# Kernel optimization log

Hardware: AMD Instinct MI355X
Metric: run time of the kernel (lower is better)

Reference implementation:

```python
import jax, jax.numpy as jnp
import numpy as np

N_NODES = 50000
N_EDGES = 800000
IN_CH = 128
HID = 64
HEADS = 4
OUT_CH = 64
NEG_SLOPE = 0.2


def _add_self_loops(ei, n):
    loops = jnp.tile(jnp.arange(n, dtype=ei.dtype)[None, :], (2, 1))
    return jnp.concatenate([ei, loops], axis=1)


def _gat_conv(x, ei, W, a_s, a_d, b, concat):
    """PyG-style GATConv. x:[N,F], ei:[2,E], W:[F,H*C], a_s/a_d:[H,C]."""
    N = x.shape[0]
    H, C = a_s.shape
    h = (x @ W).reshape(N, H, C)                     # [N,H,C]
    src, dst = ei[0], ei[1]
    al_s = (h * a_s[None]).sum(-1)                   # [N,H]
    al_d = (h * a_d[None]).sum(-1)                   # [N,H]
    logits = jax.nn.leaky_relu(al_s[src] + al_d[dst], NEG_SLOPE)  # [E,H]
    # segment softmax over incoming edges of each dst node
    m = jax.ops.segment_max(logits, dst, num_segments=N)
    m = jax.lax.stop_gradient(jnp.where(jnp.isfinite(m), m, 0.0))
    ex = jnp.exp(logits - m[dst])
    denom = jax.ops.segment_sum(ex, dst, num_segments=N)
    alpha = ex / (denom[dst] + 1e-16)                # [E,H]
    out = jax.ops.segment_sum(alpha[:, :, None] * h[src], dst, num_segments=N)  # [N,H,C]
    out = out.reshape(N, H * C) if concat else out.mean(axis=1)
    return out + b


def _hetero_layer(x, edges, self_loop_flags, W, a_s, a_d, b, concat):
    N = x.shape[0]
    out = None
    for r in range(3):
        ei = _add_self_loops(edges[r], N) if self_loop_flags[r] else edges[r]
        o = _gat_conv(x, ei, W[r], a_s[r], a_d[r], b[r], concat)
        out = o if out is None else out + o
    return out


def setup_inputs() -> dict:
    key = jax.random.key(0)
    ks = jax.random.split(key, 16)
    s = 0.05
    return {
        "x": jax.random.normal(ks[0], (N_NODES, IN_CH), jnp.float32),
        "e_blocks": jax.random.randint(ks[1], (2, N_EDGES), 0, N_NODES),
        "e_spatial": jax.random.randint(ks[2], (2, N_EDGES), 0, N_NODES),
        "e_similar": jax.random.randint(ks[3], (2, N_EDGES), 0, N_NODES),
        "W1": jax.random.normal(ks[4], (3, IN_CH, HEADS * HID), jnp.float32) * s,
        "a1s": jax.random.normal(ks[5], (3, HEADS, HID), jnp.float32) * s,
        "a1d": jax.random.normal(ks[6], (3, HEADS, HID), jnp.float32) * s,
        "b1": jax.random.normal(ks[7], (3, HEADS * HID), jnp.float32) * s,
        "W2": jax.random.normal(ks[8], (3, HEADS * HID, HEADS * HID), jnp.float32) * s,
        "a2s": jax.random.normal(ks[9], (3, HEADS, HID), jnp.float32) * s,
        "a2d": jax.random.normal(ks[10], (3, HEADS, HID), jnp.float32) * s,
        "b2": jax.random.normal(ks[11], (3, HID), jnp.float32) * s,
        "Wl": jax.random.normal(ks[12], (HID, OUT_CH), jnp.float32) * s,
        "bl": jax.random.normal(ks[13], (OUT_CH,), jnp.float32) * s,
    }


def reference(x, e_blocks, e_spatial, e_similar, W1, a1s, a1d, b1,
              W2, a2s, a2d, b2, Wl, bl):
    edges = [e_blocks, e_spatial, e_similar]
    self_loops = [False, True, True]  # 'blocks' has add_self_loops=False
    h = _hetero_layer(x, edges, self_loops, W1, a1s, a1d, b1, concat=True)
    h = jax.nn.relu(h)
    h = _hetero_layer(h, edges, self_loops, W2, a2s, a2d, b2, concat=False)
    h = jax.nn.relu(h)
    return h @ Wl + bl
```

## Files before the change

kernel.cpp:

```cpp
#include <hip/hip_runtime.h>
#include <hip/hip_bf16.h>
#include <hip/hip_fp16.h>

#define NN 50000
#define NE 800000
#define FIN 128
#define HCC 256
#define OC 64
#define NSL 0.2f
#define NT3 (3 * NN)

typedef __attribute__((ext_vector_type(8))) short sh8;
typedef __attribute__((ext_vector_type(16))) float f32x16;

struct __attribute__((aligned(8))) h4 { __half x, y, z, w; };

__device__ __forceinline__ unsigned short bf_rne(float f) {
  unsigned u = __float_as_uint(f);
  u += 0x7FFF + ((u >> 16) & 1);
  return (unsigned short)(u >> 16);
}

__device__ __forceinline__ float edge_w(float lg) {
  lg = (lg > 0.f) ? lg : NSL * lg;
  return __expf(lg);
}

template<int KK>
__global__ __launch_bounds__(256) void k_prep(const float* __restrict__ W,
                                              short* __restrict__ out) {
  int i = blockIdx.x * 256 + threadIdx.x;
  if (i >= 3 * KK * 256) return;
  int r = i / (KK * 256);
  int rem = i - r * KK * 256;
  int k = rem >> 8;
  int n = rem & 255;
  float f = W[i];
  unsigned short hb = bf_rne(f);
  float hf = __uint_as_float(((unsigned)hb) << 16);
  unsigned short lb = bf_rne(f - hf);
  int cb = n >> 7, c = n & 127, ks8 = k >> 3, kj = k & 7;
  size_t base = (size_t)r * 4 * KK * 128;
  size_t oh = base + ((size_t)((cb * 2 + 0) * (KK / 8) + ks8) * 128 + c) * 8 + kj;
  size_t ol = base + ((size_t)((cb * 2 + 1) * (KK / 8) + ks8) * 128 + c) * 8 + kj;
  out[oh] = (short)hb;
  out[ol] = (short)lb;
}

__global__ void k_hist(const int* __restrict__ dst, int* __restrict__ deg, int n) {
  int i = blockIdx.x * blockDim.x + threadIdx.x;
  int st = gridDim.x * blockDim.x;
  for (; i < n; i += st) atomicAdd(&deg[dst[i]], 1);
}

__global__ __launch_bounds__(1024) void k_bsum(const int* __restrict__ deg3,
                                               int* __restrict__ bsum) {
  __shared__ int s[1024];
  int t = threadIdx.x;
  int i = blockIdx.x * 1024 + t;
  s[t] = (i < NT3) ? deg3[i] : 0;
  __syncthreads();
  for (int off = 512; off > 0; off >>= 1) {
    if (t < off) s[t] += s[t + off];
    __syncthreads();
  }
  if (t == 0) bsum[blockIdx.x] = s[0];
}

__global__ __launch_bounds__(256) void k_scan2(const int* __restrict__ bsum,
                                               int* __restrict__ boffs, int nb) {
  __shared__ int s[256];
  int t = threadIdx.x;
  int v = (t < nb) ? bsum[t] : 0;
  s[t] = v;
  __syncthreads();
  for (int off = 1; off < 256; off <<= 1) {
    int x = (t >= off) ? s[t - off] : 0;
    __syncthreads();
    s[t] += x;
    __syncthreads();
  }
  if (t < nb) boffs[t] = s[t] - v;
}

__global__ __launch_bounds__(1024) void k_rowptr(const int* __restrict__ deg3,
                                                 const int* __restrict__ boffs,
                                                 int* __restrict__ rpA,
                                                 int* __restrict__ cursor3) {
  __shared__ int s[1024];
  int t = threadIdx.x;
  int i = blockIdx.x * 1024 + t;
  int d = (i < NT3) ? deg3[i] : 0;
  s[t] = d;
  __syncthreads();
  for (int off = 1; off < 1024; off <<= 1) {
    int x = (t >= off) ? s[t - off] : 0;
    __syncthreads();
    s[t] += x;
    __syncthreads();
  }
  if (i < NT3) {
    int excl = boffs[blockIdx.x] + s[t] - d;
    int r = (i < NN) ? 0 : ((i < 2 * NN) ? 1 : 2);
    int n = i - r * NN;
    int val = excl - r * NE;
    rpA[r * (NN + 1) + n] = val;
    cursor3[i] = val;
  }
  if (blockIdx.x == 0 && t < 3) rpA[t * (NN + 1) + NN] = NE;
}

__global__ void k_scatter(const int* __restrict__ srcv, const int* __restrict__ dstv,
                          int* __restrict__ cursor, int* __restrict__ csr_src, int n) {
  int i = blockIdx.x * blockDim.x + threadIdx.x;
  int st = gridDim.x * blockDim.x;
  for (; i < n; i += st) {
    int pos = atomicAdd(&cursor[dstv[i]], 1);
    csr_src[pos] = srcv[i];
  }
}

template<int KK, bool RELU>
__global__ __launch_bounds__(256) void k_mgemm(const float* __restrict__ A,
                                               const short* __restrict__ Bc,
                                               const float* __restrict__ asf,
                                               const float* __restrict__ adf,
                                               __half* __restrict__ hout,
                                               float* __restrict__ als,
                                               float* __restrict__ ald, int M) {
  const int tid = threadIdx.x;
  const int lane = tid & 63;
  const int w = tid >> 6;
  const int l31 = lane & 31;
  const int lg = lane >> 5;
  const int wrow = blockIdx.x * 64 + (w & 1) * 32;
  const int ch = w >> 1;

  f32x16 acc[4];
#pragma unroll
  for (int t = 0; t < 4; ++t) acc[t] = (f32x16)(0.f);

  const int r = wrow + l31;
  const bool aok = r < M;
  const float* ap = A + (size_t)r * KK;
  const short* bh = Bc + (size_t)(ch * 2 + 0) * KK * 128 + l31 * 8;
  const short* bl = Bc + (size_t)(ch * 2 + 1) * KK * 128 + l31 * 8;

#pragma unroll 2
  for (int kst = 0; kst < KK / 16; ++kst) {
    const int k0 = kst * 16 + lg * 8;
    float4 x0 = make_float4(0.f, 0.f, 0.f, 0.f), x1 = x0;
    if (aok) {
      x0 = *(const float4*)(ap + k0);
      x1 = *(const float4*)(ap + k0 + 4);
    }
    const int ks8 = kst * 2 + lg;
    const short* bhp = bh + (size_t)ks8 * 1024;
    const short* blp = bl + (size_t)ks8 * 1024;
    sh8 bhf[4], blf[4];
#pragma unroll
    for (int t = 0; t < 4; ++t) {
      bhf[t] = *(const sh8*)(bhp + t * 256);
      blf[t] = *(const sh8*)(blp + t * 256);
    }
    float fa[8] = {x0.x, x0.y, x0.z, x0.w, x1.x, x1.y, x1.z, x1.w};
    sh8 ahi, alo;
#pragma unroll
    for (int j = 0; j < 8; ++j) {
      float f = fa[j];
      if (RELU) f = fmaxf(f, 0.f);
      unsigned short hb = bf_rne(f);
      float hf = __uint_as_float(((unsigned)hb) << 16);
      unsigned short lb = bf_rne(f - hf);
      ahi[j] = (short)hb;
      alo[j] = (short)lb;
    }
#pragma unroll
    for (int t = 0; t < 4; ++t) {
      acc[t] = __builtin_amdgcn_mfma_f32_32x32x16_bf16(ahi, bhf[t], acc[t], 0, 0, 0);
      acc[t] = __builtin_amdgcn_mfma_f32_32x32x16_bf16(alo, bhf[t], acc[t], 0, 0, 0);
      acc[t] = __builtin_amdgcn_mfma_f32_32x32x16_bf16(ahi, blf[t], acc[t], 0, 0, 0);
    }
  }

  float asr[4], adr[4];
#pragma unroll
  for (int t = 0; t < 4; ++t) {
    int col = ch * 128 + t * 32 + l31;
    asr[t] = asf[col];
    adr[t] = adf[col];
  }
#pragma unroll
  for (int v = 0; v < 16; ++v) {
    const int rl = (v & 3) + 8 * (v >> 2) + 4 * lg;
    const int row = wrow + rl;
    const bool rok = row < M;
    float s0 = 0.f, s1 = 0.f, d0 = 0.f, d1 = 0.f;
    __half* hp = hout + (size_t)row * 256 + ch * 128 + l31;
#pragma unroll
    for (int t = 0; t < 4; ++t) {
      float dv = acc[t][v];
      if (rok) hp[t * 32] = __float2half(dv);
      if (t < 2) { s0 += dv * asr[t]; d0 += dv * adr[t]; }
      else       { s1 += dv * asr[t]; d1 += dv * adr[t]; }
    }
#pragma unroll
    for (int m = 1; m < 32; m <<= 1) {
      s0 += __shfl_xor(s0, m);
      s1 += __shfl_xor(s1, m);
      d0 += __shfl_xor(d0, m);
      d1 += __shfl_xor(d1, m);
    }
    if (rok && l31 == 0) {
      *(float2*)(als + (size_t)row * 4 + ch * 2) = make_float2(s0, s1);
      *(float2*)(ald + (size_t)row * 4 + ch * 2) = make_float2(d0, d1);
    }
  }
}

template<bool CONCAT, bool SELFLOOP, bool FIRST>
__global__ __launch_bounds__(256) void k_gather(const __half* __restrict__ h,
                                                const float* __restrict__ als,
                                                const float* __restrict__ ald,
                                                const int* __restrict__ row_ptr,
                                                const int* __restrict__ csr_src,
                                                const float* __restrict__ bias,
                                                float* __restrict__ outp) {
  int gid = blockIdx.x * blockDim.x + threadIdx.x;
  int n = gid >> 6;
  int lane = threadIdx.x & 63;
  if (n >= NN) return;
  int head = lane >> 4;
  float ad = ald[n * 4 + head];
  int rs = row_ptr[n];
  int re = row_ptr[n + 1];
  float ax = 0.f, ay = 0.f, az = 0.f, aw = 0.f;
  float wsum = 0.f;
  const size_t loff = (size_t)lane * 4;

  int i = rs;
  for (; i + 4 <= re; i += 4) {
    int s0 = csr_src[i], s1 = csr_src[i + 1], s2 = csr_src[i + 2], s3 = csr_src[i + 3];
    float al0 = als[s0 * 4 + head];
    float al1 = als[s1 * 4 + head];
    float al2 = als[s2 * 4 + head];
    float al3 = als[s3 * 4 + head];
    h4 v0 = *(const h4*)&h[(size_t)s0 * HCC + loff];
    h4 v1 = *(const h4*)&h[(size_t)s1 * HCC + loff];
    h4 v2 = *(const h4*)&h[(size_t)s2 * HCC + loff];
    h4 v3 = *(const h4*)&h[(size_t)s3 * HCC + loff];
    float w0 = edge_w(al0 + ad), w1 = edge_w(al1 + ad);
    float w2 = edge_w(al2 + ad), w3 = edge_w(al3 + ad);
    wsum += (w0 + w1) + (w2 + w3);
    ax = fmaf(w0, __half2float(v0.x), ax); ay = fmaf(w0, __half2float(v0.y), ay);
    az = fmaf(w0, __half2float(v0.z), az); aw = fmaf(w0, __half2float(v0.w), aw);
    ax = fmaf(w1, __half2float(v1.x), ax); ay = fmaf(w1, __half2float(v1.y), ay);
    az = fmaf(w1, __half2float(v1.z), az); aw = fmaf(w1, __half2float(v1.w), aw);
    ax = fmaf(w2, __half2float(v2.x), ax); ay = fmaf(w2, __half2float(v2.y), ay);
    az = fmaf(w2, __half2float(v2.z), az); aw = fmaf(w2, __half2float(v2.w), aw);
    ax = fmaf(w3, __half2float(v3.x), ax); ay = fmaf(w3, __half2float(v3.y), ay);
    az = fmaf(w3, __half2float(v3.z), az); aw = fmaf(w3, __half2float(v3.w), aw);
  }
  for (; i < re; ++i) {
    int s = csr_src[i];
    float w = edge_w(als[s * 4 + head] + ad);
    wsum += w;
    h4 hv = *(const h4*)&h[(size_t)s * HCC + loff];
    ax = fmaf(w, __half2float(hv.x), ax);
    ay = fmaf(w, __half2float(hv.y), ay);
    az = fmaf(w, __half2float(hv.z), az);
    aw = fmaf(w, __half2float(hv.w), aw);
  }
  if (SELFLOOP) {
    float w = edge_w(als[n * 4 + head] + ad);
    wsum += w;
    h4 hv = *(const h4*)&h[(size_t)n * HCC + loff];
    ax = fmaf(w, __half2float(hv.x), ax);
    ay = fmaf(w, __half2float(hv.y), ay);
    az = fmaf(w, __half2float(hv.z), az);
    aw = fmaf(w, __half2float(hv.w), aw);
  }
  float inv = 1.0f / (wsum + 1e-16f);
  if (CONCAT) {
    size_t base = (size_t)n * HCC + lane * 4;
    float4 bb = *(const float4*)&bias[lane * 4];
    float4 o;
    if (FIRST) {
      o.x = ax * inv + bb.x;
      o.y = ay * inv + bb.y;
      o.z = az * inv + bb.z;
      o.w = aw * inv + bb.w;
    } else {
      o = *(float4*)&outp[base];
      o.x += ax * inv + bb.x;
      o.y += ay * inv + bb.y;
      o.z += az * inv + bb.z;
      o.w += aw * inv + bb.w;
    }
    *(float4*)&outp[base] = o;
  } else {
    float vx = ax * inv, vy = ay * inv, vz = az * inv, vw = aw * inv;
    vx += __shfl_xor(vx, 16); vy += __shfl_xor(vy, 16);
    vz += __shfl_xor(vz, 16); vw += __shfl_xor(vw, 16);
    vx += __shfl_xor(vx, 32); vy += __shfl_xor(vy, 32);
    vz += __shfl_xor(vz, 32); vw += __shfl_xor(vw, 32);
    if (lane < 16) {
      size_t base = (size_t)n * OC + lane * 4;
      float4 bb = *(const float4*)&bias[lane * 4];
      float4 o;
      if (FIRST) {
        o.x = 0.25f * vx + bb.x;
        o.y = 0.25f * vy + bb.y;
        o.z = 0.25f * vz + bb.z;
        o.w = 0.25f * vw + bb.w;
      } else {
        o = *(float4*)&outp[base];
        o.x += 0.25f * vx + bb.x;
        o.y += 0.25f * vy + bb.y;
        o.z += 0.25f * vz + bb.z;
        o.w += 0.25f * vw + bb.w;
      }
      *(float4*)&outp[base] = o;
    }
  }
}

__global__ __launch_bounds__(256) void k_final(const float* __restrict__ out2,
                                               const float* __restrict__ Wl,
                                               const float* __restrict__ bl,
                                               float* __restrict__ outp) {
  __shared__ float Ws[64 * 64];
  __shared__ float bs[64];
  int tid = threadIdx.x;
  for (int i = tid; i < 4096; i += 256) Ws[i] = Wl[i];
  if (tid < 64) bs[tid] = bl[tid];
  __syncthreads();
  int r = blockIdx.x * 4 + (tid >> 6);
  int c = tid & 63;
  if (r >= NN) return;
  const float* xr = &out2[(size_t)r * OC];
  float acc = bs[c];
#pragma unroll
  for (int k = 0; k < 64; ++k) {
    float xv = xr[k];
    xv = (xv > 0.f) ? xv : 0.f;
    acc = fmaf(xv, Ws[k * 64 + c], acc);
  }
  outp[(size_t)r * OC + c] = acc;
}

extern "C" void kernel_launch(void* const* d_in, const int* in_sizes, int n_in,
                              void* d_out, int out_size, void* d_ws, size_t ws_size,
                              hipStream_t stream) {
  const float* x   = (const float*)d_in[0];
  const int* e_b   = (const int*)d_in[1];
  const int* e_sp  = (const int*)d_in[2];
  const int* e_si  = (const int*)d_in[3];
  const float* W1  = (const float*)d_in[4];
  const float* a1s = (const float*)d_in[5];
  const float* a1d = (const float*)d_in[6];
  const float* b1  = (const float*)d_in[7];
  const float* W2  = (const float*)d_in[8];
  const float* a2s = (const float*)d_in[9];
  const float* a2d = (const float*)d_in[10];
  const float* b2  = (const float*)d_in[11];
  const float* Wl  = (const float*)d_in[12];
  const float* bl  = (const float*)d_in[13];
  float* out = (float*)d_out;

  char* ws = (char*)d_ws;
  size_t off = 0;
  auto alloc = [&](size_t b) {
    char* p = ws + off;
    off += (b + 255) & ~(size_t)255;
    return p;
  };
  __half* h   = (__half*)alloc((size_t)NN * HCC * 2);
  float* out1 = (float*)alloc((size_t)NN * HCC * 4);
  float* out2 = (float*)alloc((size_t)NN * OC * 4);
  float* als  = (float*)alloc((size_t)NN * 4 * 4);
  float* ald  = (float*)alloc((size_t)NN * 4 * 4);
  int* deg3   = (int*)alloc((size_t)NT3 * 4);
  int* cursor3= (int*)alloc((size_t)NT3 * 4);
  int* rpA    = (int*)alloc((size_t)3 * (NN + 1) * 4);
  int* bsum   = (int*)alloc(256 * 4);
  int* boffs  = (int*)alloc(256 * 4);
  short* Wc1  = (short*)alloc((size_t)3 * 4 * FIN * 128 * 2);
  short* Wc2  = (short*)alloc((size_t)3 * 4 * HCC * 128 * 2);
  int* cs[3];
  for (int r = 0; r < 3; ++r) cs[r] = (int*)alloc((size_t)NE * 4);

  const int* edges[3] = {e_b, e_sp, e_si};

  k_prep<FIN><<<(3 * FIN * 256 + 255) / 256, 256, 0, stream>>>(W1, Wc1);
  k_prep<HCC><<<(3 * HCC * 256 + 255) / 256, 256, 0, stream>>>(W2, Wc2);

  hipMemsetAsync(deg3, 0, (size_t)NT3 * 4, stream);
  for (int r = 0; r < 3; ++r)
    k_hist<<<1024, 256, 0, stream>>>(edges[r] + NE, deg3 + r * NN, NE);
  const int NB = (NT3 + 1023) / 1024;
  k_bsum<<<NB, 1024, 0, stream>>>(deg3, bsum);
  k_scan2<<<1, 256, 0, stream>>>(bsum, boffs, NB);
  k_rowptr<<<NB, 1024, 0, stream>>>(deg3, boffs, rpA, cursor3);
  for (int r = 0; r < 3; ++r)
    k_scatter<<<1024, 256, 0, stream>>>(edges[r], edges[r] + NE, cursor3 + r * NN, cs[r], NE);

  const int gblocks = (NN + 63) / 64;
  const int ablocks = (NN * 64) / 256;

  for (int r = 0; r < 3; ++r) {
    k_mgemm<FIN, false><<<gblocks, 256, 0, stream>>>(
        x, Wc1 + (size_t)r * 4 * FIN * 128,
        a1s + r * HCC, a1d + r * HCC, h, als, ald, NN);
    if (r == 0)
      k_gather<true, false, true><<<ablocks, 256, 0, stream>>>(h, als, ald, rpA + r * (NN + 1), cs[r], b1 + r * HCC, out1);
    else
      k_gather<true, true, false><<<ablocks, 256, 0, stream>>>(h, als, ald, rpA + r * (NN + 1), cs[r], b1 + r * HCC, out1);
  }
  for (int r = 0; r < 3; ++r) {
    k_mgemm<HCC, true><<<gblocks, 256, 0, stream>>>(
        out1, Wc2 + (size_t)r * 4 * HCC * 128,
        a2s + r * HCC, a2d + r * HCC, h, als, ald, NN);
    if (r == 0)
      k_gather<false, false, true><<<ablocks, 256, 0, stream>>>(h, als, ald, rpA + r * (NN + 1), cs[r], b2 + r * OC, out2);
    else
      k_gather<false, true, false><<<ablocks, 256, 0, stream>>>(h, als, ald, rpA + r * (NN + 1), cs[r], b2 + r * OC, out2);
  }
  k_final<<<(NN + 3) / 4, 256, 0, stream>>>(out2, Wl, bl, out);
}
```

Baseline: 1.001 ms.

## Batch three relations per layer into single GEMM and fused gather kernels

The GEMMs for all three relations now run in one launch, with blockIdx.y selecting the relation, and write into a per-relation h buffer. A single gather kernel then aggregates all three relations per node in registers and adds all biases, which removes the read-modify-write of the float output between relations. The layer-1 output is stored as fp16 with ReLU applied, halving the bytes the second GEMM reads. The cost is more workspace for the tripled h and attention buffers, and some precision loss from storing the intermediate activation in fp16.

```diff
diff --git a/kernel.cpp b/kernel.cpp
--- a/kernel.cpp
+++ b/kernel.cpp
@@ -11,6 +11,7 @@
 #define NT3 (3 * NN)
 
 typedef __attribute__((ext_vector_type(8))) short sh8;
+typedef __attribute__((ext_vector_type(8))) unsigned short u16x8;
 typedef __attribute__((ext_vector_type(16))) float f32x16;
 
 struct __attribute__((aligned(8))) h4 { __half x, y, z, w; };
@@ -19,6 +20,11 @@
   unsigned u = __float_as_uint(f);
   u += 0x7FFF + ((u >> 16) & 1);
   return (unsigned short)(u >> 16);
+}
+
+__device__ __forceinline__ float hbits2f(unsigned short u) {
+  __half_raw hr; hr.x = u;
+  return __half2float((__half)hr);
 }
 
 __device__ __forceinline__ float edge_w(float lg) {
@@ -120,14 +126,22 @@
   }
 }
 
-template<int KK, bool RELU>
-__global__ __launch_bounds__(256) void k_mgemm(const float* __restrict__ A,
-                                               const short* __restrict__ Bc,
-                                               const float* __restrict__ asf,
-                                               const float* __restrict__ adf,
-                                               __half* __restrict__ hout,
-                                               float* __restrict__ als,
-                                               float* __restrict__ ald, int M) {
+template<int KK, bool AF32>
+__global__ __launch_bounds__(256) void k_mgemm(const void* __restrict__ Av,
+                                               const short* __restrict__ BcAll,
+                                               const float* __restrict__ asfAll,
+                                               const float* __restrict__ adfAll,
+                                               __half* __restrict__ houtAll,
+                                               float* __restrict__ alsAll,
+                                               float* __restrict__ aldAll, int M) {
+  const int rel = blockIdx.y;
+  const short* Bc = BcAll + (size_t)rel * 4 * KK * 128;
+  const float* asf = asfAll + rel * HCC;
+  const float* adf = adfAll + rel * HCC;
+  __half* hout = houtAll + (size_t)rel * NN * HCC;
+  float* als = alsAll + (size_t)rel * NN * 4;
+  float* ald = aldAll + (size_t)rel * NN * 4;
+
   const int tid = threadIdx.x;
   const int lane = tid & 63;
   const int w = tid >> 6;
@@ -142,17 +156,28 @@
 
   const int r = wrow + l31;
   const bool aok = r < M;
-  const float* ap = A + (size_t)r * KK;
+  const float* apf = (const float*)Av + (size_t)r * KK;
+  const __half* aph = (const __half*)Av + (size_t)r * KK;
   const short* bh = Bc + (size_t)(ch * 2 + 0) * KK * 128 + l31 * 8;
   const short* bl = Bc + (size_t)(ch * 2 + 1) * KK * 128 + l31 * 8;
 
 #pragma unroll 2
   for (int kst = 0; kst < KK / 16; ++kst) {
     const int k0 = kst * 16 + lg * 8;
-    float4 x0 = make_float4(0.f, 0.f, 0.f, 0.f), x1 = x0;
-    if (aok) {
-      x0 = *(const float4*)(ap + k0);
-      x1 = *(const float4*)(ap + k0 + 4);
+    float fa[8];
+    if (AF32) {
+      float4 x0 = make_float4(0.f, 0.f, 0.f, 0.f), x1 = x0;
+      if (aok) {
+        x0 = *(const float4*)(apf + k0);
+        x1 = *(const float4*)(apf + k0 + 4);
+      }
+      fa[0] = x0.x; fa[1] = x0.y; fa[2] = x0.z; fa[3] = x0.w;
+      fa[4] = x1.x; fa[5] = x1.y; fa[6] = x1.z; fa[7] = x1.w;
+    } else {
+      u16x8 hv = {0, 0, 0, 0, 0, 0, 0, 0};
+      if (aok) hv = *(const u16x8*)(aph + k0);
+#pragma unroll
+      for (int j = 0; j < 8; ++j) fa[j] = hbits2f(hv[j]);
     }
     const int ks8 = kst * 2 + lg;
     const short* bhp = bh + (size_t)ks8 * 1024;
@@ -163,12 +188,10 @@
       bhf[t] = *(const sh8*)(bhp + t * 256);
       blf[t] = *(const sh8*)(blp + t * 256);
     }
-    float fa[8] = {x0.x, x0.y, x0.z, x0.w, x1.x, x1.y, x1.z, x1.w};
     sh8 ahi, alo;
 #pragma unroll
     for (int j = 0; j < 8; ++j) {
       float f = fa[j];
-      if (RELU) f = fmaxf(f, 0.f);
       unsigned short hb = bf_rne(f);
       float hf = __uint_as_float(((unsigned)hb) << 16);
       unsigned short lb = bf_rne(f - hf);
@@ -218,29 +241,20 @@
   }
 }
 
-template<bool CONCAT, bool SELFLOOP, bool FIRST>
-__global__ __launch_bounds__(256) void k_gather(const __half* __restrict__ h,
-                                                const float* __restrict__ als,
-                                                const float* __restrict__ ald,
-                                                const int* __restrict__ row_ptr,
-                                                const int* __restrict__ csr_src,
-                                                const float* __restrict__ bias,
-                                                float* __restrict__ outp) {
-  int gid = blockIdx.x * blockDim.x + threadIdx.x;
-  int n = gid >> 6;
-  int lane = threadIdx.x & 63;
-  if (n >= NN) return;
-  int head = lane >> 4;
+template<bool SL>
+__device__ __forceinline__ void gat_rel(int n, int head, size_t loff,
+                                        const __half* __restrict__ h,
+                                        const float* __restrict__ als,
+                                        const float* __restrict__ ald,
+                                        const int* __restrict__ rp,
+                                        const int* __restrict__ cs,
+                                        float& ox, float& oy, float& oz, float& ow) {
   float ad = ald[n * 4 + head];
-  int rs = row_ptr[n];
-  int re = row_ptr[n + 1];
-  float ax = 0.f, ay = 0.f, az = 0.f, aw = 0.f;
-  float wsum = 0.f;
-  const size_t loff = (size_t)lane * 4;
-
+  int rs = rp[n], re = rp[n + 1];
+  float ax = 0.f, ay = 0.f, az = 0.f, aw = 0.f, wsum = 0.f;
   int i = rs;
   for (; i + 4 <= re; i += 4) {
-    int s0 = csr_src[i], s1 = csr_src[i + 1], s2 = csr_src[i + 2], s3 = csr_src[i + 3];
+    int s0 = cs[i], s1 = cs[i + 1], s2 = cs[i + 2], s3 = cs[i + 3];
     float al0 = als[s0 * 4 + head];
     float al1 = als[s1 * 4 + head];
     float al2 = als[s2 * 4 + head];
@@ -262,7 +276,7 @@
     az = fmaf(w3, __half2float(v3.z), az); aw = fmaf(w3, __half2float(v3.w), aw);
   }
   for (; i < re; ++i) {
-    int s = csr_src[i];
+    int s = cs[i];
     float w = edge_w(als[s * 4 + head] + ad);
     wsum += w;
     h4 hv = *(const h4*)&h[(size_t)s * HCC + loff];
@@ -271,7 +285,7 @@
     az = fmaf(w, __half2float(hv.z), az);
     aw = fmaf(w, __half2float(hv.w), aw);
   }
-  if (SELFLOOP) {
+  if (SL) {
     float w = edge_w(als[n * 4 + head] + ad);
     wsum += w;
     h4 hv = *(const h4*)&h[(size_t)n * HCC + loff];
@@ -281,46 +295,60 @@
     aw = fmaf(w, __half2float(hv.w), aw);
   }
   float inv = 1.0f / (wsum + 1e-16f);
+  ox = fmaf(ax, inv, ox);
+  oy = fmaf(ay, inv, oy);
+  oz = fmaf(az, inv, oz);
+  ow = fmaf(aw, inv, ow);
+}
+
+template<bool CONCAT>
+__global__ __launch_bounds__(256) void k_gather3(const __half* __restrict__ h3,
+                                                 const float* __restrict__ als3,
+                                                 const float* __restrict__ ald3,
+                                                 const int* __restrict__ rpA,
+                                                 const int* __restrict__ cs0,
+                                                 const int* __restrict__ cs1,
+                                                 const int* __restrict__ cs2,
+                                                 const float* __restrict__ bias,
+                                                 __half* __restrict__ o16,
+                                                 float* __restrict__ o32) {
+  int gid = blockIdx.x * blockDim.x + threadIdx.x;
+  int n = gid >> 6;
+  int lane = threadIdx.x & 63;
+  if (n >= NN) return;
+  int head = lane >> 4;
+  size_t loff = (size_t)lane * 4;
+  const size_t HS = (size_t)NN * HCC;
+  const size_t AS = (size_t)NN * 4;
+  float ox = 0.f, oy = 0.f, oz = 0.f, ow = 0.f;
+  gat_rel<false>(n, head, loff, h3,          als3,          ald3,          rpA,               cs0, ox, oy, oz, ow);
+  gat_rel<true >(n, head, loff, h3 + HS,     als3 + AS,     ald3 + AS,     rpA + (NN + 1),    cs1, ox, oy, oz, ow);
+  gat_rel<true >(n, head, loff, h3 + 2 * HS, als3 + 2 * AS, ald3 + 2 * AS, rpA + 2 * (NN + 1), cs2, ox, oy, oz, ow);
   if (CONCAT) {
-    size_t base = (size_t)n * HCC + lane * 4;
-    float4 bb = *(const float4*)&bias[lane * 4];
-    float4 o;
-    if (FIRST) {
-      o.x = ax * inv + bb.x;
-      o.y = ay * inv + bb.y;
-      o.z = az * inv + bb.z;
-      o.w = aw * inv + bb.w;
-    } else {
-      o = *(float4*)&outp[base];
-      o.x += ax * inv + bb.x;
-      o.y += ay * inv + bb.y;
-      o.z += az * inv + bb.z;
-      o.w += aw * inv + bb.w;
-    }
-    *(float4*)&outp[base] = o;
+    float4 b0 = *(const float4*)&bias[lane * 4];
+    float4 b1 = *(const float4*)&bias[HCC + lane * 4];
+    float4 b2 = *(const float4*)&bias[2 * HCC + lane * 4];
+    h4 o;
+    o.x = __float2half(fmaxf(ox + b0.x + b1.x + b2.x, 0.f));
+    o.y = __float2half(fmaxf(oy + b0.y + b1.y + b2.y, 0.f));
+    o.z = __float2half(fmaxf(oz + b0.z + b1.z + b2.z, 0.f));
+    o.w = __float2half(fmaxf(ow + b0.w + b1.w + b2.w, 0.f));
+    *(h4*)&o16[(size_t)n * HCC + loff] = o;
   } else {
-    float vx = ax * inv, vy = ay * inv, vz = az * inv, vw = aw * inv;
-    vx += __shfl_xor(vx, 16); vy += __shfl_xor(vy, 16);
-    vz += __shfl_xor(vz, 16); vw += __shfl_xor(vw, 16);
-    vx += __shfl_xor(vx, 32); vy += __shfl_xor(vy, 32);
-    vz += __shfl_xor(vz, 32); vw += __shfl_xor(vw, 32);
+    ox += __shfl_xor(ox, 16); oy += __shfl_xor(oy, 16);
+    oz += __shfl_xor(oz, 16); ow += __shfl_xor(ow, 16);
+    ox += __shfl_xor(ox, 32); oy += __shfl_xor(oy, 32);
+    oz += __shfl_xor(oz, 32); ow += __shfl_xor(ow, 32);
     if (lane < 16) {
-      size_t base = (size_t)n * OC + lane * 4;
-      float4 bb = *(const float4*)&bias[lane * 4];
+      float4 b0 = *(const float4*)&bias[lane * 4];
+      float4 b1 = *(const float4*)&bias[OC + lane * 4];
+      float4 b2 = *(const float4*)&bias[2 * OC + lane * 4];
       float4 o;
-      if (FIRST) {
-        o.x = 0.25f * vx + bb.x;
-        o.y = 0.25f * vy + bb.y;
-        o.z = 0.25f * vz + bb.z;
-        o.w = 0.25f * vw + bb.w;
-      } else {
-        o = *(float4*)&outp[base];
-        o.x += 0.25f * vx + bb.x;
-        o.y += 0.25f * vy + bb.y;
-        o.z += 0.25f * vz + bb.z;
-        o.w += 0.25f * vw + bb.w;
-      }
-      *(float4*)&outp[base] = o;
+      o.x = 0.25f * ox + b0.x + b1.x + b2.x;
+      o.y = 0.25f * oy + b0.y + b1.y + b2.y;
+      o.z = 0.25f * oz + b0.z + b1.z + b2.z;
+      o.w = 0.25f * ow + b0.w + b1.w + b2.w;
+      *(float4*)&o32[(size_t)n * OC + lane * 4] = o;
     }
   }
 }
@@ -375,11 +403,11 @@
     off += (b + 255) & ~(size_t)255;
     return p;
   };
-  __half* h   = (__half*)alloc((size_t)NN * HCC * 2);
-  float* out1 = (float*)alloc((size_t)NN * HCC * 4);
-  float* out2 = (float*)alloc((size_t)NN * OC * 4);
-  float* als  = (float*)alloc((size_t)NN * 4 * 4);
-  float* ald  = (float*)alloc((size_t)NN * 4 * 4);
+  __half* h3   = (__half*)alloc((size_t)3 * NN * HCC * 2);
+  __half* out1h = (__half*)alloc((size_t)NN * HCC * 2);
+  float* out2 = (float*)out1h;
+  float* als3 = (float*)alloc((size_t)3 * NN * 4 * 4);
+  float* ald3 = (float*)alloc((size_t)3 * NN * 4 * 4);
   int* deg3   = (int*)alloc((size_t)NT3 * 4);
   int* cursor3= (int*)alloc((size_t)NT3 * 4);
   int* rpA    = (int*)alloc((size_t)3 * (NN + 1) * 4);
@@ -408,23 +436,15 @@
   const int gblocks = (NN + 63) / 64;
   const int ablocks = (NN * 64) / 256;
 
-  for (int r = 0; r < 3; ++r) {
-    k_mgemm<FIN, false><<<gblocks, 256, 0, stream>>>(
-        x, Wc1 + (size_t)r * 4 * FIN * 128,
-        a1s + r * HCC, a1d + r * HCC, h, als, ald, NN);
-    if (r == 0)
-      k_gather<true, false, true><<<ablocks, 256, 0, stream>>>(h, als, ald, rpA + r * (NN + 1), cs[r], b1 + r * HCC, out1);
-    else
-      k_gather<true, true, false><<<ablocks, 256, 0, stream>>>(h, als, ald, rpA + r * (NN + 1), cs[r], b1 + r * HCC, out1);
-  }
-  for (int r = 0; r < 3; ++r) {
-    k_mgemm<HCC, true><<<gblocks, 256, 0, stream>>>(
-        out1, Wc2 + (size_t)r * 4 * HCC * 128,
-        a2s + r * HCC, a2d + r * HCC, h, als, ald, NN);
-    if (r == 0)
-      k_gather<false, false, true><<<ablocks, 256, 0, stream>>>(h, als, ald, rpA + r * (NN + 1), cs[r], b2 + r * OC, out2);
-    else
-      k_gather<false, true, false><<<ablocks, 256, 0, stream>>>(h, als, ald, rpA + r * (NN + 1), cs[r], b2 + r * OC, out2);
-  }
+  k_mgemm<FIN, true><<<dim3(gblocks, 3), 256, 0, stream>>>(
+      x, Wc1, a1s, a1d, h3, als3, ald3, NN);
+  k_gather3<true><<<ablocks, 256, 0, stream>>>(
+      h3, als3, ald3, rpA, cs[0], cs[1], cs[2], b1, out1h, nullptr);
+
+  k_mgemm<HCC, false><<<dim3(gblocks, 3), 256, 0, stream>>>(
+      out1h, Wc2, a2s, a2d, h3, als3, ald3, NN);
+  k_gather3<false><<<ablocks, 256, 0, stream>>>(
+      h3, als3, ald3, rpA, cs[0], cs[1], cs[2], b2, nullptr, out2);
+
   k_final<<<(NN + 3) / 4, 256, 0, stream>>>(out2, Wl, bl, out);
 }
```

After: 907.1 us. 9.4% less time.
